# Optimization experiments

Hardware: AMD Instinct MI355X
Metric: run time of the kernel (lower is better)

## Reference

```python
import jax, jax.numpy as jnp
import numpy as np

B, S, E, H, D = 64, 512, 512, 8, 64  # batch, n_steps, embedding_size, head_count, QKV_dim

def setup_inputs() -> dict:
    key = jax.random.key(0)
    ks = jax.random.split(key, 7)
    x = jax.random.normal(ks[0], (B, S, E), dtype=jnp.float32)
    mask = jax.random.randint(ks[1], (B, S), 0, 2).astype(jnp.float32)  # 1 = masked out
    WQ = jax.random.normal(ks[2], (H, E, D), dtype=jnp.float32) * 0.1
    WK = jax.random.normal(ks[3], (H, E, D), dtype=jnp.float32) * 0.1
    WV = jax.random.normal(ks[4], (H, E, D), dtype=jnp.float32) * 0.1
    BE = jax.random.normal(ks[5], (S, E), dtype=jnp.float32) * 0.1
    WO = jax.random.normal(ks[6], (H * D, E), dtype=jnp.float32) * 0.1
    return {"x": x, "mask": mask, "WQ": WQ, "WK": WK, "WV": WV, "BE": BE, "WO": WO}

def reference(x, mask, WQ, WK, WV, BE, WO):
    # add learned positional bias
    h = x + BE  # [B,S,E]
    # per-head projections, vectorized over heads
    Q = jnp.einsum('bse,hed->bhsd', h, WQ)
    K = jnp.einsum('bse,hed->bhsd', h, WK)
    V = jnp.einsum('bse,hed->bhsd', h, WV)
    # NOTE: original scales by sqrt(embedding_size), not sqrt(QKV_dim)
    scores = jnp.einsum('bhsd,bhtd->bhst', Q, K) / np.sqrt(E).astype(np.float32)
    # additive mask trick: mask tiled over query dim, key positions masked where mask==1
    scores = scores - mask[:, None, None, :] * 1e10
    alpha = jax.nn.softmax(scores, axis=-1)  # [B,H,S,S]
    attn = jnp.einsum('bhst,bhtd->bhsd', alpha, V)  # [B,H,S,D]
    # concat heads along feature dim -> [B,S,H*D], then output projection
    attn = jnp.transpose(attn, (0, 2, 1, 3)).reshape(x.shape[0], x.shape[1], -1)
    return attn @ WO  # [B,S,E]
```

## Files before the change

kernel.cpp:

```cpp
#include <hip/hip_runtime.h>
#include <hip/hip_bf16.h>


#define Bn 64
#define Sn 512
#define En 512
#define Hn 8
#define Dn 64

typedef __attribute__((ext_vector_type(8))) short s8v;
typedef __attribute__((ext_vector_type(4))) float f4v;

__device__ __forceinline__ unsigned short f2bf(float f) {
    union { float f; unsigned int u; } v; v.f = f;
    unsigned int u = v.u;
    u += 0x7fffu + ((u >> 16) & 1u);
    return (unsigned short)(u >> 16);
}

__device__ __forceinline__ void async16(const unsigned short* g, unsigned short* l) {
    __builtin_amdgcn_global_load_lds((const __attribute__((address_space(1))) void*)g,
                                     (__attribute__((address_space(3))) void*)l, 16, 0, 0);
}
__device__ __forceinline__ void async4(const float* g, float* l) {
    __builtin_amdgcn_global_load_lds((const __attribute__((address_space(1))) void*)g,
                                     (__attribute__((address_space(3))) void*)l, 4, 0, 0);
}

__global__ __launch_bounds__(256) void prep_h(const float* __restrict__ x,
                                              const float* __restrict__ BE,
                                              unsigned short* __restrict__ hbf) {
    int i = (blockIdx.x * 256 + threadIdx.x) * 4;
    int se = i % (Sn * En);
    float4 a = *(const float4*)(x + i);
    float4 b = *(const float4*)(BE + se);
    ushort4 o;
    o.x = f2bf(a.x + b.x); o.y = f2bf(a.y + b.y);
    o.z = f2bf(a.z + b.z); o.w = f2bf(a.w + b.w);
    *(ushort4*)(hbf + i) = o;
}

__global__ __launch_bounds__(256) void prep_w(const float* __restrict__ WQ,
                                              const float* __restrict__ WK,
                                              const float* __restrict__ WV,
                                              const float* __restrict__ WO,
                                              unsigned short* __restrict__ Wqkvt,
                                              unsigned short* __restrict__ WOt) {
    int idx = blockIdx.x * 256 + threadIdx.x;
    const int NW = 3 * Hn * Dn * En;
    if (idx < NW) {
        int e = idx & 511;
        int d = (idx >> 9) & 63;
        int h = (idx >> 15) & 7;
        int m = idx >> 18;
        const float* W = (m == 0) ? WQ : (m == 1) ? WK : WV;
        Wqkvt[idx] = f2bf(W[(h * En + e) * Dn + d]);
    } else {
        int j = idx - NW;
        int n = j & 511;
        int e = j >> 9;
        WOt[j] = f2bf(WO[n * En + e]);
    }
}

__device__ __forceinline__ void mfma8(const s8v& a0k0, const s8v& a0k1,
                                      const s8v& a1k0, const s8v& a1k1,
                                      f4v* acc0, f4v* acc1,
                                      const s8v (&bq)[4][2], bool sw) {
    if (sw) {
#pragma unroll
        for (int n = 0; n < 4; n++) {
            acc0[n] = __builtin_amdgcn_mfma_f32_16x16x32_bf16(bq[n][0], a0k0, acc0[n], 0, 0, 0);
            acc0[n] = __builtin_amdgcn_mfma_f32_16x16x32_bf16(bq[n][1], a0k1, acc0[n], 0, 0, 0);
            acc1[n] = __builtin_amdgcn_mfma_f32_16x16x32_bf16(bq[n][0], a1k0, acc1[n], 0, 0, 0);
            acc1[n] = __builtin_amdgcn_mfma_f32_16x16x32_bf16(bq[n][1], a1k1, acc1[n], 0, 0, 0);
        }
    } else {
#pragma unroll
        for (int n = 0; n < 4; n++) {
            acc0[n] = __builtin_amdgcn_mfma_f32_16x16x32_bf16(a0k0, bq[n][0], acc0[n], 0, 0, 0);
            acc0[n] = __builtin_amdgcn_mfma_f32_16x16x32_bf16(a0k1, bq[n][1], acc0[n], 0, 0, 0);
            acc1[n] = __builtin_amdgcn_mfma_f32_16x16x32_bf16(a1k0, bq[n][0], acc1[n], 0, 0, 0);
            acc1[n] = __builtin_amdgcn_mfma_f32_16x16x32_bf16(a1k1, bq[n][1], acc1[n], 0, 0, 0);
        }
    }
}

__global__ __launch_bounds__(512, 2) void qkv_gemm(const unsigned short* __restrict__ hbf,
                                                   const unsigned short* __restrict__ Wqkvt,
                                                   unsigned short* __restrict__ Qo,
                                                   unsigned short* __restrict__ Ko,
                                                   unsigned short* __restrict__ Vt) {
    __shared__ __align__(16) unsigned short As[2][16384];
    __shared__ __align__(16) unsigned short Bs[2][16384];

    int lin = blockIdx.y * 6 + blockIdx.x;
    int swz = (lin & 7) * 96 + (lin >> 3);
    int mb = swz / 6, nbv = swz - mb * 6;

    int tid = threadIdx.x;
    int w = tid >> 6, lane = tid & 63, quad = lane >> 4, l16 = lane & 15, l7 = l16 & 7;
    int wr = w >> 2, wcn = w & 3;

    const unsigned short* Ag = hbf + (size_t)mb * 256 * 512;
    const unsigned short* Bg = Wqkvt + (size_t)nbv * 256 * 512;

    int colbase = nbv * 256 + wcn * 64;
    bool swapQK = colbase < 1024;

    int ha = (lane >> 3) & 1;
    int ca = w * 4 + (lane >> 4);
    int aG0 = (ca + 128 * ha) * 512 + ((lane & 7) ^ (ca & 7)) * 8;
    int rb0 = w * 8 + (lane >> 3);
    int bG0 = rb0 * 512 + ((lane & 7) ^ (rb0 & 7)) * 8;

    int arow = 2 * l16 + wr;
    int aseg0 = (quad ^ l7) * 8;
    int aseg1 = ((4 + quad) ^ l7) * 8;

    f4v acc[8][4];
#pragma unroll
    for (int i = 0; i < 8; i++)
#pragma unroll
        for (int n = 0; n < 4; n++) acc[i][n] = (f4v){0.f, 0.f, 0.f, 0.f};
    s8v bq[4][2];

#define STA8(o_, p_, kt_) async16(Ag + aG0 + (p_) * 16384 + (kt_) * 64, &As[o_][(p_) * 4096 + w * 512])
#define STB8(o_, q_, kt_) async16(Bg + bG0 + (q_) * 32768 + (kt_) * 64, &Bs[o_][(q_) * 4096 + w * 512])

#define PHASE8(P, STAGES, GATE)                                                   \
    do {                                                                          \
        if ((P) == 0) {                                                           \
            _Pragma("unroll")                                                     \
            for (int n = 0; n < 4; n++) {                                         \
                int br = (wcn * 64 + n * 16 + l16) * 64;                          \
                bq[n][0] = *(const s8v*)&Bs_s[br + aseg0];                        \
                bq[n][1] = *(const s8v*)&Bs_s[br + aseg1];                        \
            }                                                                     \
        }                                                                         \
        s8v a0k0 = *(const s8v*)&As_s[(((P) * 2 + 0) * 32 + arow) * 64 + aseg0];  \
        s8v a0k1 = *(const s8v*)&As_s[(((P) * 2 + 0) * 32 + arow) * 64 + aseg1];  \
        s8v a1k0 = *(const s8v*)&As_s[(((P) * 2 + 1) * 32 + arow) * 64 + aseg0];  \
        s8v a1k1 = *(const s8v*)&As_s[(((P) * 2 + 1) * 32 + arow) * 64 + aseg1];  \
        STAGES;                                                                   \
        __builtin_amdgcn_s_barrier();                                             \
        asm volatile("s_waitcnt lgkmcnt(0)" ::: "memory");                        \
        __builtin_amdgcn_s_setprio(1);                                            \
        mfma8(a0k0, a0k1, a1k0, a1k1, &acc[(P) * 2][0], &acc[(P) * 2 + 1][0], bq, swapQK); \
        __builtin_amdgcn_s_setprio(0);                                            \
        GATE;                                                                     \
        __builtin_amdgcn_s_barrier();                                             \
    } while (0)

    STB8(0, 0, 0); STB8(0, 1, 0); STB8(0, 2, 0); STB8(0, 3, 0);
    STA8(0, 0, 0); STA8(0, 1, 0); STA8(0, 2, 0); STA8(0, 3, 0);
    asm volatile("s_waitcnt vmcnt(0)" ::: "memory");
    __builtin_amdgcn_s_barrier();

    for (int k = 0; k < 7; k++) {
        int s = k & 1, o = s ^ 1, kt = k + 1;
        const unsigned short* As_s = &As[s][0];
        const unsigned short* Bs_s = &Bs[s][0];
        PHASE8(0, { STB8(o, 0, kt); STB8(o, 1, kt); STA8(o, 0, kt); },
               asm volatile("s_waitcnt vmcnt(6)" ::: "memory"));
        PHASE8(1, { STB8(o, 2, kt); STA8(o, 1, kt); },
               asm volatile("s_waitcnt vmcnt(6)" ::: "memory"));
        PHASE8(2, { STB8(o, 3, kt); STA8(o, 2, kt); },
               asm volatile("s_waitcnt vmcnt(7)" ::: "memory"));
        PHASE8(3, { STA8(o, 3, kt); },
               asm volatile("s_waitcnt vmcnt(2)" ::: "memory"));
    }
    {
        const unsigned short* As_s = &As[1][0];
        const unsigned short* Bs_s = &Bs[1][0];
        PHASE8(0, {}, asm volatile("s_waitcnt vmcnt(3)" ::: "memory"));
        PHASE8(1, {}, asm volatile("s_waitcnt vmcnt(1)" ::: "memory"));
        PHASE8(2, {}, asm volatile("s_waitcnt vmcnt(0)" ::: "memory"));
        PHASE8(3, {}, (void)0);
    }
#undef PHASE8
#undef STA8
#undef STB8

    int mat = colbase >> 9;
    int h = (colbase >> 6) & 7;
    int b_idx = mb >> 1;
    const float qscale = 0.06375873f;

    if (swapQK) {
        unsigned short* op = (mat == 0) ? Qo : Ko;
        float sc = (mat == 0) ? qscale : 1.0f;
#pragma unroll
        for (int mi = 0; mi < 8; mi++)
#pragma unroll
            for (int n = 0; n < 4; n++) {
                int s_ = (mb & 1) * 256 + wr * 128 + mi * 16 + l16;
                int d0 = n * 16 + quad * 4;
                ushort4 pk;
                pk.x = f2bf(acc[mi][n][0] * sc);
                pk.y = f2bf(acc[mi][n][1] * sc);
                pk.z = f2bf(acc[mi][n][2] * sc);
                pk.w = f2bf(acc[mi][n][3] * sc);
                *(ushort4*)&op[(size_t)((b_idx * Hn + h) * Sn + s_) * Dn + d0] = pk;
            }
    } else {
#pragma unroll
        for (int mi = 0; mi < 8; mi++)
#pragma unroll
            for (int n = 0; n < 4; n++) {
                int d = n * 16 + l16;
                int srow = (mb & 1) * 256 + wr * 128 + mi * 16 + quad * 4;
                ushort4 pk;
                pk.x = f2bf(acc[mi][n][0]); pk.y = f2bf(acc[mi][n][1]);
                pk.z = f2bf(acc[mi][n][2]); pk.w = f2bf(acc[mi][n][3]);
                *(ushort4*)&Vt[(size_t)((b_idx * Hn + h) * Dn + d) * Sn + srow] = pk;
            }
    }
}

__global__ __launch_bounds__(256) void attn_kernel(const unsigned short* __restrict__ Q,
                                                   const unsigned short* __restrict__ K,
                                                   const unsigned short* __restrict__ Vt,
                                                   const float* __restrict__ mask,
                                                   unsigned short* __restrict__ attn) {
    int qhalf = blockIdx.x, bh = blockIdx.y;
    int h = bh & 7, b = bh >> 3;
    __shared__ __align__(16) unsigned short Kc[64 * 64];
    __shared__ __align__(16) unsigned short Vc[64 * 64];
    __shared__ __align__(16) unsigned short Ps[4][4 * 16 * 64];
    __shared__ float maskv[64];
    int tid = threadIdx.x;
    int w = tid >> 6, lane = tid & 63, quad = lane >> 4, l16 = lane & 15;
    int l7 = l16 & 7;

    const unsigned short* Qg = Q + (size_t)(bh * Sn + qhalf * 256) * Dn;
    const unsigned short* Kg = K + (size_t)(bh * Sn) * Dn;
    const unsigned short* Vg = Vt + (size_t)(bh * Dn) * Sn;

    s8v aq[4][2];
#pragma unroll
    for (int i = 0; i < 4; i++)
#pragma unroll
        for (int ks = 0; ks < 2; ks++)
            aq[i][ks] = *(const s8v*)&Qg[((w * 4 + i) * 16 + l16) * 64 + ks * 32 + quad * 8];

    f4v acc[4][4];
    float psum[4] = {0.f, 0.f, 0.f, 0.f};
#pragma unroll
    for (int i = 0; i < 4; i++)
#pragma unroll
        for (int n = 0; n < 4; n++) acc[i][n] = (f4v){0.f, 0.f, 0.f, 0.f};

    int srow0 = w * 16 + (lane >> 3);
    int srow1 = srow0 + 8;
    int gseg0 = ((lane & 7) ^ (srow0 & 7)) * 8;
    int gseg1 = ((lane & 7) ^ (srow1 & 7)) * 8;
    unsigned short* kdst0 = &Kc[(w * 16) * 64];
    unsigned short* kdst1 = &Kc[(w * 16 + 8) * 64];
    unsigned short* vdst0 = &Vc[(w * 16) * 64];
    unsigned short* vdst1 = &Vc[(w * 16 + 8) * 64];

    unsigned short* Pw = Ps[w];
    int wbase = l16 * 64 + (quad & 1) * 4;
    const float cM = -1.4426950409e10f;

    for (int kc = 0; kc < 8; kc++) {
        __syncthreads();
        async16(Kg + (kc * 64 + srow0) * 64 + gseg0, kdst0);
        async16(Kg + (kc * 64 + srow1) * 64 + gseg1, kdst1);
        async16(Vg + srow0 * 512 + kc * 64 + gseg0, vdst0);
        async16(Vg + srow1 * 512 + kc * 64 + gseg1, vdst1);
        if (w == 0) async4(mask + b * Sn + kc * 64 + lane, maskv);
        __syncthreads();

#pragma unroll
        for (int n = 0; n < 4; n++) {
            s8v bk0 = *(const s8v*)&Kc[(n * 16 + l16) * 64 + (quad ^ l7) * 8];
            s8v bk1 = *(const s8v*)&Kc[(n * 16 + l16) * 64 + ((4 + quad) ^ l7) * 8];
            float4 mv = *(const float4*)&maskv[n * 16 + quad * 4];
            float m0 = mv.x * cM, m1 = mv.y * cM, m2 = mv.z * cM, m3 = mv.w * cM;
            int wseg = ((n * 2 + (quad >> 1)) ^ l7) * 8;
            f4v sacc[4];
#pragma unroll
            for (int i = 0; i < 4; i++) {
                sacc[i] = __builtin_amdgcn_mfma_f32_16x16x32_bf16(
                              bk0, aq[i][0], (f4v){0.f, 0.f, 0.f, 0.f}, 0, 0, 0);
                sacc[i] = __builtin_amdgcn_mfma_f32_16x16x32_bf16(
                              bk1, aq[i][1], sacc[i], 0, 0, 0);
            }
#pragma unroll
            for (int i = 0; i < 4; i++) {
                unsigned int u0 = __float_as_uint(__builtin_amdgcn_exp2f(sacc[i][0] + m0));
                unsigned int u1 = __float_as_uint(__builtin_amdgcn_exp2f(sacc[i][1] + m1));
                unsigned int u2 = __float_as_uint(__builtin_amdgcn_exp2f(sacc[i][2] + m2));
                unsigned int u3 = __float_as_uint(__builtin_amdgcn_exp2f(sacc[i][3] + m3));
                psum[i] += __uint_as_float(u0 & 0xffff0000u) + __uint_as_float(u1 & 0xffff0000u)
                         + __uint_as_float(u2 & 0xffff0000u) + __uint_as_float(u3 & 0xffff0000u);
                uint2 pk;
                pk.x = (u0 >> 16) | (u1 & 0xffff0000u);
                pk.y = (u2 >> 16) | (u3 & 0xffff0000u);
                *(uint2*)&Pw[(i << 10) + wbase + wseg] = pk;
            }
        }

#pragma unroll
        for (int ks = 0; ks < 2; ks++) {
            int sw = ((ks * 4 + quad) ^ l7) * 8;
            s8v ap[4];
#pragma unroll
            for (int i = 0; i < 4; i++)
                ap[i] = *(const s8v*)&Pw[(i << 10) + l16 * 64 + sw];
#pragma unroll
            for (int n = 0; n < 4; n++) {
                s8v bv = *(const s8v*)&Vc[(n * 16 + l16) * 64 + sw];
#pragma unroll
                for (int i = 0; i < 4; i++)
                    acc[i][n] = __builtin_amdgcn_mfma_f32_16x16x32_bf16(ap[i], bv, acc[i][n], 0, 0, 0);
            }
        }
    }

#pragma unroll
    for (int i = 0; i < 4; i++) {
        float s = psum[i];
        s += __shfl_xor(s, 16, 64);
        s += __shfl_xor(s, 32, 64);
        float inv[4];
#pragma unroll
        for (int r = 0; r < 4; r++)
            inv[r] = 1.0f / __shfl(s, quad * 4 + r, 64);
#pragma unroll
        for (int n = 0; n < 4; n++)
#pragma unroll
            for (int r = 0; r < 4; r++) {
                int query = qhalf * 256 + (w * 4 + i) * 16 + quad * 4 + r;
                int col = h * 64 + n * 16 + l16;
                attn[(size_t)(b * Sn + query) * (Hn * Dn) + col] = f2bf(acc[i][n][r] * inv[r]);
            }
    }
}

__global__ __launch_bounds__(256) void outproj(const unsigned short* __restrict__ attn,
                                               const unsigned short* __restrict__ WOt,
                                               float* __restrict__ out) {
    int nb = blockIdx.x, mb = blockIdx.y;
    __shared__ __align__(16) unsigned short At[2][128 * 64];
    __shared__ __align__(16) unsigned short Bt[2][128 * 64];
    int tid = threadIdx.x;
    int w = tid >> 6, lane = tid & 63, quad = lane >> 4, l16 = lane & 15;
    int wr = w >> 1, wc = w & 1;
    int lrow = lane >> 3;
    int lseg = ((lane & 7) ^ lrow) * 8;

    f4v acc[4][4];
#pragma unroll
    for (int i = 0; i < 4; i++)
#pragma unroll
        for (int n = 0; n < 4; n++) acc[i][n] = (f4v){0.f, 0.f, 0.f, 0.f};

    const unsigned short* Ag = attn + (size_t)mb * 128 * 512;
    const unsigned short* Bg = WOt + (size_t)nb * 128 * 512;

#pragma unroll
    for (int i = 0; i < 4; i++) {
        int r0 = w * 32 + i * 8;
        async16(Ag + (r0 + lrow) * 512 + lseg, &At[0][r0 * 64]);
        async16(Bg + (r0 + lrow) * 512 + lseg, &Bt[0][r0 * 64]);
    }

    int cur = 0;
    for (int kc = 0; kc < 8; kc++) {
        if (kc < 7) {
            int nxt = cur ^ 1;
#pragma unroll
            for (int i = 0; i < 4; i++) {
                int r0 = w * 32 + i * 8;
                async16(Ag + (r0 + lrow) * 512 + (kc + 1) * 64 + lseg, &At[nxt][r0 * 64]);
                async16(Bg + (r0 + lrow) * 512 + (kc + 1) * 64 + lseg, &Bt[nxt][r0 * 64]);
            }
            asm volatile("s_waitcnt vmcnt(8)" ::: "memory");
        } else {
            asm volatile("s_waitcnt vmcnt(0)" ::: "memory");
        }
        __builtin_amdgcn_s_barrier();

#pragma unroll
        for (int ks = 0; ks < 2; ks++) {
            int sw = ((ks * 4 + quad) ^ (l16 & 7)) * 8;
            s8v a[4], b[4];
#pragma unroll
            for (int i = 0; i < 4; i++)
                a[i] = *(const s8v*)&At[cur][(wr * 64 + i * 16 + l16) * 64 + sw];
#pragma unroll
            for (int n = 0; n < 4; n++)
                b[n] = *(const s8v*)&Bt[cur][(wc * 64 + n * 16 + l16) * 64 + sw];
#pragma unroll
            for (int i = 0; i < 4; i++)
#pragma unroll
                for (int n = 0; n < 4; n++)
                    acc[i][n] = __builtin_amdgcn_mfma_f32_16x16x32_bf16(b[n], a[i], acc[i][n], 0, 0, 0);
        }
        asm volatile("s_waitcnt lgkmcnt(0)" ::: "memory");
        __builtin_amdgcn_s_barrier();
        cur ^= 1;
    }
#pragma unroll
    for (int i = 0; i < 4; i++)
#pragma unroll
        for (int n = 0; n < 4; n++) {
            int row = mb * 128 + wr * 64 + i * 16 + l16;
            int col = nb * 128 + wc * 64 + n * 16 + quad * 4;
            float4 o;
            o.x = acc[i][n][0]; o.y = acc[i][n][1];
            o.z = acc[i][n][2]; o.w = acc[i][n][3];
            *(float4*)&out[(size_t)row * 512 + col] = o;
        }
}

extern "C" void kernel_launch(void* const* d_in, const int* in_sizes, int n_in,
                              void* d_out, int out_size, void* d_ws, size_t ws_size,
                              hipStream_t stream) {
    const float* x    = (const float*)d_in[0];
    const float* mask = (const float*)d_in[1];
    const float* WQ   = (const float*)d_in[2];
    const float* WK   = (const float*)d_in[3];
    const float* WV   = (const float*)d_in[4];
    const float* BE   = (const float*)d_in[5];
    const float* WO   = (const float*)d_in[6];
    float* out = (float*)d_out;

    char* ws = (char*)d_ws;
    unsigned short* hbf   = (unsigned short*)(ws);
    unsigned short* Wqkvt = (unsigned short*)(ws + 33554432);
    unsigned short* WOt   = (unsigned short*)(ws + 35127296);
    unsigned short* Qp    = (unsigned short*)(ws + 35651584);
    unsigned short* Kp    = (unsigned short*)(ws + 69206016);
    unsigned short* Vtp   = (unsigned short*)(ws + 102760448);
    unsigned short* attnp = (unsigned short*)(ws + 136314880);

    prep_h<<<16384, 256, 0, stream>>>(x, BE, hbf);
    prep_w<<<4096, 256, 0, stream>>>(WQ, WK, WV, WO, Wqkvt, WOt);
    qkv_gemm<<<dim3(6, 128), 512, 0, stream>>>(hbf, Wqkvt, Qp, Kp, Vtp);
    attn_kernel<<<dim3(2, 512), 256, 0, stream>>>(Qp, Kp, Vtp, mask, attnp);
    outproj<<<dim3(4, 256), 256, 0, stream>>>(attnp, WOt, out);
}
```

Measured before the change: 292.0 us.

## Double-buffer K/V tiles in attention kernel and preload the full mask row

The attention kernel now keeps two LDS buffers for the K and V chunks. It prefetches chunk kc+1 with async global-to-LDS loads while computing chunk kc, replacing the old pattern of barrier, load, barrier on every iteration. The whole 512-entry mask row for the batch is loaded into shared memory once up front. The output-projection GEMM swaps its manual vmcnt waits and raw barriers for __syncthreads. This costs more LDS per block, which may reduce occupancy.

```diff
diff --git a/kernel.cpp b/kernel.cpp
--- a/kernel.cpp
+++ b/kernel.cpp
@@ -225,10 +225,10 @@
                                                    unsigned short* __restrict__ attn) {
     int qhalf = blockIdx.x, bh = blockIdx.y;
     int h = bh & 7, b = bh >> 3;
-    __shared__ __align__(16) unsigned short Kc[64 * 64];
-    __shared__ __align__(16) unsigned short Vc[64 * 64];
+    __shared__ __align__(16) unsigned short Kc[2][64 * 64];
+    __shared__ __align__(16) unsigned short Vc[2][64 * 64];
     __shared__ __align__(16) unsigned short Ps[4][4 * 16 * 64];
-    __shared__ float maskv[64];
+    __shared__ float maskv[512];
     int tid = threadIdx.x;
     int w = tid >> 6, lane = tid & 63, quad = lane >> 4, l16 = lane & 15;
     int l7 = l16 & 7;
@@ -255,29 +255,39 @@
     int srow1 = srow0 + 8;
     int gseg0 = ((lane & 7) ^ (srow0 & 7)) * 8;
     int gseg1 = ((lane & 7) ^ (srow1 & 7)) * 8;
-    unsigned short* kdst0 = &Kc[(w * 16) * 64];
-    unsigned short* kdst1 = &Kc[(w * 16 + 8) * 64];
-    unsigned short* vdst0 = &Vc[(w * 16) * 64];
-    unsigned short* vdst1 = &Vc[(w * 16 + 8) * 64];
+    int kd0 = (w * 16) * 64, kd1 = (w * 16 + 8) * 64;
 
     unsigned short* Pw = Ps[w];
     int wbase = l16 * 64 + (quad & 1) * 4;
     const float cM = -1.4426950409e10f;
 
+    async16(Kg + srow0 * 64 + gseg0, &Kc[0][kd0]);
+    async16(Kg + srow1 * 64 + gseg1, &Kc[0][kd1]);
+    async16(Vg + srow0 * 512 + gseg0, &Vc[0][kd0]);
+    async16(Vg + srow1 * 512 + gseg1, &Vc[0][kd1]);
+    async4(mask + b * Sn + w * 128 + lane, &maskv[w * 128]);
+    async4(mask + b * Sn + w * 128 + 64 + lane, &maskv[w * 128 + 64]);
+    asm volatile("s_waitcnt vmcnt(0)" ::: "memory");
+    __builtin_amdgcn_s_barrier();
+
     for (int kc = 0; kc < 8; kc++) {
-        __syncthreads();
-        async16(Kg + (kc * 64 + srow0) * 64 + gseg0, kdst0);
-        async16(Kg + (kc * 64 + srow1) * 64 + gseg1, kdst1);
-        async16(Vg + srow0 * 512 + kc * 64 + gseg0, vdst0);
-        async16(Vg + srow1 * 512 + kc * 64 + gseg1, vdst1);
-        if (w == 0) async4(mask + b * Sn + kc * 64 + lane, maskv);
-        __syncthreads();
+        int cur = kc & 1, nxt = cur ^ 1;
+        if (kc < 7) {
+            async16(Kg + ((kc + 1) * 64 + srow0) * 64 + gseg0, &Kc[nxt][kd0]);
+            async16(Kg + ((kc + 1) * 64 + srow1) * 64 + gseg1, &Kc[nxt][kd1]);
+            async16(Vg + srow0 * 512 + (kc + 1) * 64 + gseg0, &Vc[nxt][kd0]);
+            async16(Vg + srow1 * 512 + (kc + 1) * 64 + gseg1, &Vc[nxt][kd1]);
+            asm volatile("s_waitcnt vmcnt(4)" ::: "memory");
+        } else {
+            asm volatile("s_waitcnt vmcnt(0)" ::: "memory");
+        }
+        __builtin_amdgcn_s_barrier();
 
 #pragma unroll
         for (int n = 0; n < 4; n++) {
-            s8v bk0 = *(const s8v*)&Kc[(n * 16 + l16) * 64 + (quad ^ l7) * 8];
-            s8v bk1 = *(const s8v*)&Kc[(n * 16 + l16) * 64 + ((4 + quad) ^ l7) * 8];
-            float4 mv = *(const float4*)&maskv[n * 16 + quad * 4];
+            s8v bk0 = *(const s8v*)&Kc[cur][(n * 16 + l16) * 64 + (quad ^ l7) * 8];
+            s8v bk1 = *(const s8v*)&Kc[cur][(n * 16 + l16) * 64 + ((4 + quad) ^ l7) * 8];
+            float4 mv = *(const float4*)&maskv[kc * 64 + n * 16 + quad * 4];
             float m0 = mv.x * cM, m1 = mv.y * cM, m2 = mv.z * cM, m3 = mv.w * cM;
             int wseg = ((n * 2 + (quad >> 1)) ^ l7) * 8;
             f4v sacc[4];
@@ -312,12 +322,14 @@
                 ap[i] = *(const s8v*)&Pw[(i << 10) + l16 * 64 + sw];
 #pragma unroll
             for (int n = 0; n < 4; n++) {
-                s8v bv = *(const s8v*)&Vc[(n * 16 + l16) * 64 + sw];
+                s8v bv = *(const s8v*)&Vc[cur][(n * 16 + l16) * 64 + sw];
 #pragma unroll
                 for (int i = 0; i < 4; i++)
                     acc[i][n] = __builtin_amdgcn_mfma_f32_16x16x32_bf16(ap[i], bv, acc[i][n], 0, 0, 0);
             }
         }
+        asm volatile("s_waitcnt lgkmcnt(0)" ::: "memory");
+        __builtin_amdgcn_s_barrier();
     }
 
 #pragma unroll
@@ -367,6 +379,7 @@
         async16(Ag + (r0 + lrow) * 512 + lseg, &At[0][r0 * 64]);
         async16(Bg + (r0 + lrow) * 512 + lseg, &Bt[0][r0 * 64]);
     }
+    __syncthreads();
 
     int cur = 0;
     for (int kc = 0; kc < 8; kc++) {
@@ -378,12 +391,7 @@
                 async16(Ag + (r0 + lrow) * 512 + (kc + 1) * 64 + lseg, &At[nxt][r0 * 64]);
                 async16(Bg + (r0 + lrow) * 512 + (kc + 1) * 64 + lseg, &Bt[nxt][r0 * 64]);
             }
-            asm volatile("s_waitcnt vmcnt(8)" ::: "memory");
-        } else {
-            asm volatile("s_waitcnt vmcnt(0)" ::: "memory");
-        }
-        __builtin_amdgcn_s_barrier();
-
+        }
 #pragma unroll
         for (int ks = 0; ks < 2; ks++) {
             int sw = ((ks * 4 + quad) ^ (l16 & 7)) * 8;
@@ -400,8 +408,7 @@
                 for (int n = 0; n < 4; n++)
                     acc[i][n] = __builtin_amdgcn_mfma_f32_16x16x32_bf16(b[n], a[i], acc[i][n], 0, 0, 0);
         }
-        asm volatile("s_waitcnt lgkmcnt(0)" ::: "memory");
-        __builtin_amdgcn_s_barrier();
+        if (kc < 7) __syncthreads();
         cur ^= 1;
     }
 #pragma unroll
```

Result: no change. 294.8 us (+1.0%).

## Retile output projection to 256x256 blocks with phased pipelining; merge prep kernels

Applied to the files above, without the earlier changes.

The two preprocessing kernels are merged into a single launch, which removes one kernel launch. The output projection GEMM moves from 128x128 tiles with 256 threads to 256x256 tiles with 512 threads and 64-wide K stages. Each stage is split into four phases that interleave async LDS loads with MFMA work, using setprio and fine-grained vmcnt waits, and the block order is swizzled. Larger tiles raise data reuse per block, but only 256 blocks are launched, which may leave some compute units underused.

```diff
diff --git a/kernel.cpp b/kernel.cpp
--- a/kernel.cpp
+++ b/kernel.cpp
@@ -27,39 +27,41 @@
                                      (__attribute__((address_space(3))) void*)l, 4, 0, 0);
 }
 
-__global__ __launch_bounds__(256) void prep_h(const float* __restrict__ x,
-                                              const float* __restrict__ BE,
-                                              unsigned short* __restrict__ hbf) {
-    int i = (blockIdx.x * 256 + threadIdx.x) * 4;
-    int se = i % (Sn * En);
-    float4 a = *(const float4*)(x + i);
-    float4 b = *(const float4*)(BE + se);
-    ushort4 o;
-    o.x = f2bf(a.x + b.x); o.y = f2bf(a.y + b.y);
-    o.z = f2bf(a.z + b.z); o.w = f2bf(a.w + b.w);
-    *(ushort4*)(hbf + i) = o;
-}
-
-__global__ __launch_bounds__(256) void prep_w(const float* __restrict__ WQ,
-                                              const float* __restrict__ WK,
-                                              const float* __restrict__ WV,
-                                              const float* __restrict__ WO,
-                                              unsigned short* __restrict__ Wqkvt,
-                                              unsigned short* __restrict__ WOt) {
-    int idx = blockIdx.x * 256 + threadIdx.x;
-    const int NW = 3 * Hn * Dn * En;
-    if (idx < NW) {
-        int e = idx & 511;
-        int d = (idx >> 9) & 63;
-        int h = (idx >> 15) & 7;
-        int m = idx >> 18;
-        const float* W = (m == 0) ? WQ : (m == 1) ? WK : WV;
-        Wqkvt[idx] = f2bf(W[(h * En + e) * Dn + d]);
+__global__ __launch_bounds__(256) void prep_all(const float* __restrict__ x,
+                                                const float* __restrict__ BE,
+                                                const float* __restrict__ WQ,
+                                                const float* __restrict__ WK,
+                                                const float* __restrict__ WV,
+                                                const float* __restrict__ WO,
+                                                unsigned short* __restrict__ hbf,
+                                                unsigned short* __restrict__ Wqkvt,
+                                                unsigned short* __restrict__ WOt) {
+    int bid = blockIdx.x;
+    if (bid < 16384) {
+        int i = (bid * 256 + threadIdx.x) * 4;
+        int se = i % (Sn * En);
+        float4 a = *(const float4*)(x + i);
+        float4 b = *(const float4*)(BE + se);
+        ushort4 o;
+        o.x = f2bf(a.x + b.x); o.y = f2bf(a.y + b.y);
+        o.z = f2bf(a.z + b.z); o.w = f2bf(a.w + b.w);
+        *(ushort4*)(hbf + i) = o;
     } else {
-        int j = idx - NW;
-        int n = j & 511;
-        int e = j >> 9;
-        WOt[j] = f2bf(WO[n * En + e]);
+        int idx = (bid - 16384) * 256 + threadIdx.x;
+        const int NW = 3 * Hn * Dn * En;
+        if (idx < NW) {
+            int e = idx & 511;
+            int d = (idx >> 9) & 63;
+            int h = (idx >> 15) & 7;
+            int m = idx >> 18;
+            const float* W = (m == 0) ? WQ : (m == 1) ? WK : WV;
+            Wqkvt[idx] = f2bf(W[(h * En + e) * Dn + d]);
+        } else {
+            int j = idx - NW;
+            int n = j & 511;
+            int e = j >> 9;
+            WOt[j] = f2bf(WO[n * En + e]);
+        }
     }
 }
 
@@ -340,79 +342,106 @@
     }
 }
 
-__global__ __launch_bounds__(256) void outproj(const unsigned short* __restrict__ attn,
-                                               const unsigned short* __restrict__ WOt,
-                                               float* __restrict__ out) {
-    int nb = blockIdx.x, mb = blockIdx.y;
-    __shared__ __align__(16) unsigned short At[2][128 * 64];
-    __shared__ __align__(16) unsigned short Bt[2][128 * 64];
+__global__ __launch_bounds__(512, 2) void outproj(const unsigned short* __restrict__ attn,
+                                                  const unsigned short* __restrict__ WOt,
+                                                  float* __restrict__ out) {
+    __shared__ __align__(16) unsigned short As[2][16384];
+    __shared__ __align__(16) unsigned short Bs[2][16384];
+
+    int lin = blockIdx.y * 2 + blockIdx.x;
+    int swz = (lin & 7) * 32 + (lin >> 3);
+    int mb = swz >> 1, nbv = swz & 1;
+
     int tid = threadIdx.x;
-    int w = tid >> 6, lane = tid & 63, quad = lane >> 4, l16 = lane & 15;
-    int wr = w >> 1, wc = w & 1;
-    int lrow = lane >> 3;
-    int lseg = ((lane & 7) ^ lrow) * 8;
-
-    f4v acc[4][4];
-#pragma unroll
-    for (int i = 0; i < 4; i++)
+    int w = tid >> 6, lane = tid & 63, quad = lane >> 4, l16 = lane & 15, l7 = l16 & 7;
+    int wr = w >> 2, wcn = w & 3;
+
+    const unsigned short* Ag = attn + (size_t)mb * 256 * 512;
+    const unsigned short* Bg = WOt + (size_t)nbv * 256 * 512;
+
+    int ha = (lane >> 3) & 1;
+    int ca = w * 4 + (lane >> 4);
+    int aG0 = (ca + 128 * ha) * 512 + ((lane & 7) ^ (ca & 7)) * 8;
+    int rb0 = w * 8 + (lane >> 3);
+    int bG0 = rb0 * 512 + ((lane & 7) ^ (rb0 & 7)) * 8;
+
+    int arow = 2 * l16 + wr;
+    int aseg0 = (quad ^ l7) * 8;
+    int aseg1 = ((4 + quad) ^ l7) * 8;
+
+    f4v acc[8][4];
+#pragma unroll
+    for (int i = 0; i < 8; i++)
 #pragma unroll
         for (int n = 0; n < 4; n++) acc[i][n] = (f4v){0.f, 0.f, 0.f, 0.f};
-
-    const unsigned short* Ag = attn + (size_t)mb * 128 * 512;
-    const unsigned short* Bg = WOt + (size_t)nb * 128 * 512;
-
-#pragma unroll
-    for (int i = 0; i < 4; i++) {
-        int r0 = w * 32 + i * 8;
-        async16(Ag + (r0 + lrow) * 512 + lseg, &At[0][r0 * 64]);
-        async16(Bg + (r0 + lrow) * 512 + lseg, &Bt[0][r0 * 64]);
-    }
-
-    int cur = 0;
-    for (int kc = 0; kc < 8; kc++) {
-        if (kc < 7) {
-            int nxt = cur ^ 1;
-#pragma unroll
-            for (int i = 0; i < 4; i++) {
-                int r0 = w * 32 + i * 8;
-                async16(Ag + (r0 + lrow) * 512 + (kc + 1) * 64 + lseg, &At[nxt][r0 * 64]);
-                async16(Bg + (r0 + lrow) * 512 + (kc + 1) * 64 + lseg, &Bt[nxt][r0 * 64]);
-            }
-            asm volatile("s_waitcnt vmcnt(8)" ::: "memory");
-        } else {
-            asm volatile("s_waitcnt vmcnt(0)" ::: "memory");
-        }
-        __builtin_amdgcn_s_barrier();
-
-#pragma unroll
-        for (int ks = 0; ks < 2; ks++) {
-            int sw = ((ks * 4 + quad) ^ (l16 & 7)) * 8;
-            s8v a[4], b[4];
-#pragma unroll
-            for (int i = 0; i < 4; i++)
-                a[i] = *(const s8v*)&At[cur][(wr * 64 + i * 16 + l16) * 64 + sw];
-#pragma unroll
-            for (int n = 0; n < 4; n++)
-                b[n] = *(const s8v*)&Bt[cur][(wc * 64 + n * 16 + l16) * 64 + sw];
-#pragma unroll
-            for (int i = 0; i < 4; i++)
-#pragma unroll
-                for (int n = 0; n < 4; n++)
-                    acc[i][n] = __builtin_amdgcn_mfma_f32_16x16x32_bf16(b[n], a[i], acc[i][n], 0, 0, 0);
-        }
-        asm volatile("s_waitcnt lgkmcnt(0)" ::: "memory");
-        __builtin_amdgcn_s_barrier();
-        cur ^= 1;
-    }
-#pragma unroll
-    for (int i = 0; i < 4; i++)
+    s8v bq[4][2];
+
+#define STA8(o_, p_, kt_) async16(Ag + aG0 + (p_) * 16384 + (kt_) * 64, &As[o_][(p_) * 4096 + w * 512])
+#define STB8(o_, q_, kt_) async16(Bg + bG0 + (q_) * 32768 + (kt_) * 64, &Bs[o_][(q_) * 4096 + w * 512])
+
+#define PHASE8(P, STAGES, GATE)                                                   \
+    do {                                                                          \
+        if ((P) == 0) {                                                           \
+            _Pragma("unroll")                                                     \
+            for (int n = 0; n < 4; n++) {                                         \
+                int br = (wcn * 64 + n * 16 + l16) * 64;                          \
+                bq[n][0] = *(const s8v*)&Bs_s[br + aseg0];                        \
+                bq[n][1] = *(const s8v*)&Bs_s[br + aseg1];                        \
+            }                                                                     \
+        }                                                                         \
+        s8v a0k0 = *(const s8v*)&As_s[(((P) * 2 + 0) * 32 + arow) * 64 + aseg0];  \
+        s8v a0k1 = *(const s8v*)&As_s[(((P) * 2 + 0) * 32 + arow) * 64 + aseg1];  \
+        s8v a1k0 = *(const s8v*)&As_s[(((P) * 2 + 1) * 32 + arow) * 64 + aseg0];  \
+        s8v a1k1 = *(const s8v*)&As_s[(((P) * 2 + 1) * 32 + arow) * 64 + aseg1];  \
+        STAGES;                                                                   \
+        __builtin_amdgcn_s_barrier();                                             \
+        asm volatile("s_waitcnt lgkmcnt(0)" ::: "memory");                        \
+        __builtin_amdgcn_s_setprio(1);                                            \
+        mfma8(a0k0, a0k1, a1k0, a1k1, &acc[(P) * 2][0], &acc[(P) * 2 + 1][0], bq, true); \
+        __builtin_amdgcn_s_setprio(0);                                            \
+        GATE;                                                                     \
+        __builtin_amdgcn_s_barrier();                                             \
+    } while (0)
+
+    STB8(0, 0, 0); STB8(0, 1, 0); STB8(0, 2, 0); STB8(0, 3, 0);
+    STA8(0, 0, 0); STA8(0, 1, 0); STA8(0, 2, 0); STA8(0, 3, 0);
+    asm volatile("s_waitcnt vmcnt(0)" ::: "memory");
+    __builtin_amdgcn_s_barrier();
+
+    for (int k = 0; k < 7; k++) {
+        int s = k & 1, o = s ^ 1, kt = k + 1;
+        const unsigned short* As_s = &As[s][0];
+        const unsigned short* Bs_s = &Bs[s][0];
+        PHASE8(0, { STB8(o, 0, kt); STB8(o, 1, kt); STA8(o, 0, kt); },
+               asm volatile("s_waitcnt vmcnt(6)" ::: "memory"));
+        PHASE8(1, { STB8(o, 2, kt); STA8(o, 1, kt); },
+               asm volatile("s_waitcnt vmcnt(6)" ::: "memory"));
+        PHASE8(2, { STB8(o, 3, kt); STA8(o, 2, kt); },
+               asm volatile("s_waitcnt vmcnt(7)" ::: "memory"));
+        PHASE8(3, { STA8(o, 3, kt); },
+               asm volatile("s_waitcnt vmcnt(2)" ::: "memory"));
+    }
+    {
+        const unsigned short* As_s = &As[1][0];
+        const unsigned short* Bs_s = &Bs[1][0];
+        PHASE8(0, {}, asm volatile("s_waitcnt vmcnt(3)" ::: "memory"));
+        PHASE8(1, {}, asm volatile("s_waitcnt vmcnt(1)" ::: "memory"));
+        PHASE8(2, {}, asm volatile("s_waitcnt vmcnt(0)" ::: "memory"));
+        PHASE8(3, {}, (void)0);
+    }
+#undef PHASE8
+#undef STA8
+#undef STB8
+
+#pragma unroll
+    for (int mi = 0; mi < 8; mi++)
 #pragma unroll
         for (int n = 0; n < 4; n++) {
-            int row = mb * 128 + wr * 64 + i * 16 + l16;
-            int col = nb * 128 + wc * 64 + n * 16 + quad * 4;
+            int row = mb * 256 + wr * 128 + mi * 16 + l16;
+            int col = nbv * 256 + wcn * 64 + n * 16 + quad * 4;
             float4 o;
-            o.x = acc[i][n][0]; o.y = acc[i][n][1];
-            o.z = acc[i][n][2]; o.w = acc[i][n][3];
+            o.x = acc[mi][n][0]; o.y = acc[mi][n][1];
+            o.z = acc[mi][n][2]; o.w = acc[mi][n][3];
             *(float4*)&out[(size_t)row * 512 + col] = o;
         }
 }
@@ -438,9 +467,8 @@
     unsigned short* Vtp   = (unsigned short*)(ws + 102760448);
     unsigned short* attnp = (unsigned short*)(ws + 136314880);
 
-    prep_h<<<16384, 256, 0, stream>>>(x, BE, hbf);
-    prep_w<<<4096, 256, 0, stream>>>(WQ, WK, WV, WO, Wqkvt, WOt);
+    prep_all<<<20480, 256, 0, stream>>>(x, BE, WQ, WK, WV, WO, hbf, Wqkvt, WOt);
     qkv_gemm<<<dim3(6, 128), 512, 0, stream>>>(hbf, Wqkvt, Qp, Kp, Vtp);
     attn_kernel<<<dim3(2, 512), 256, 0, stream>>>(Qp, Kp, Vtp, mask, attnp);
-    outproj<<<dim3(4, 256), 256, 0, stream>>>(attnp, WOt, out);
-}
+    outproj<<<dim3(2, 128), 512, 0, stream>>>(attnp, WOt, out);
+}
```

New measurement: 287.1 us. No clear change (-1.7%).
